# Kernel tuning notes

Measured on AMD Instinct MI355X. Metric: run time of the kernel, lower is better.

Reference implementation:

```python
import jax, jax.numpy as jnp
import numpy as np

B, N, M, D, H, K, V = 2, 2048, 2048, 1024, 16, 64, 64
MAX_WAVELENGTH = 10000
SCALE_FACTOR = 1.0


def rope(x, positions, max_wavelength, scale_factor):
    # x: [b, s, h, k]; positions: [b, s] int
    head_dim = x.shape[-1]
    fraction = 2.0 * jnp.arange(head_dim // 2, dtype=x.dtype) / head_dim
    timescale = jnp.asarray(max_wavelength, x.dtype) ** fraction            # [k/2]
    # scaled positions -> phase per (b, s, 1 head bcast, k/2)
    phase = (positions.astype(x.dtype) / scale_factor)[:, :, None, None] / timescale  # [b,s,1,k/2]
    sin, cos = jnp.sin(phase), jnp.cos(phase)
    x1, x2 = jnp.split(x, 2, axis=-1)
    return jnp.concatenate([x1 * cos - x2 * sin, x2 * cos + x1 * sin], axis=-1)


def setup_inputs() -> dict:
    key = jax.random.key(0)
    ks = jax.random.split(key, 8)
    scale = 1.0 / np.sqrt(D)  # keep logits numerically sane with random params
    inp = {
        "query": jax.random.normal(ks[0], (B, N, D), jnp.float32),
        "q_positions": jnp.broadcast_to(jnp.arange(N, dtype=jnp.int32), (B, N)),
        "key": jax.random.normal(ks[1], (B, M, D), jnp.float32),
        "k_positions": jnp.broadcast_to(jnp.arange(M, dtype=jnp.int32), (B, M)),
        "value": jax.random.normal(ks[2], (B, M, D), jnp.float32),
        "mask": jnp.ones((1, 1, N, M), dtype=bool),
        "P_q": jax.random.normal(ks[3], (H, D, K), jnp.float32) * scale,
        "P_k": jax.random.normal(ks[4], (H, D, K), jnp.float32) * scale,
        "P_v": jax.random.normal(ks[5], (H, D, V), jnp.float32) * scale,
        "P_o": jax.random.normal(ks[6], (H, D, V), jnp.float32) * scale,
    }
    return inp


def reference(query, q_positions, key, k_positions, value, mask, P_q, P_k, P_v, P_o):
    q = jnp.einsum('bnd,hdk->bnhk', query, P_q)
    k = jnp.einsum('bmd,hdk->bmhk', key, P_k)
    v = jnp.einsum('bmd,hdv->bmhv', value, P_v)
    q = rope(q, q_positions, MAX_WAVELENGTH, SCALE_FACTOR)
    k = rope(k, k_positions, MAX_WAVELENGTH, SCALE_FACTOR)
    logits = jnp.einsum('bnhk,bmhk->bhnm', q, k)
    if mask is not None:
        logits = jnp.where(mask, logits, -jnp.inf)
    weights = jax.nn.softmax(logits, axis=-1)
    o = jnp.einsum('bhnm,bmhv->bnhv', weights, v)
    return jnp.einsum('bnhv,hdv->bnd', o, P_o)
```

## Files before the change

### kernel.cpp

```cpp
#include <hip/hip_runtime.h>
#include <hip/hip_bf16.h>
#include <math.h>

#define B_ 2
#define N_ 2048
#define M_ 2048
#define D_ 1024
#define H_ 16


typedef _Float16 f16;
typedef f16  f16x4 __attribute__((ext_vector_type(4)));
typedef f16  f16x8 __attribute__((ext_vector_type(8)));
typedef float f32x4  __attribute__((ext_vector_type(4)));
typedef float f32x16 __attribute__((ext_vector_type(16)));

#define MFMA16(a, b, c) __builtin_amdgcn_mfma_f32_16x16x32_f16((a), (b), (c), 0, 0, 0)
#define MFMA32(a, b, c) __builtin_amdgcn_mfma_f32_32x32x16_f16((a), (b), (c), 0, 0, 0)
#define LDST 72

static __device__ __forceinline__ unsigned int pk2(float a, float b) {
  auto h = __builtin_amdgcn_cvt_pkrtz(a, b);
  return __builtin_bit_cast(unsigned int, h);
}

__global__ __launch_bounds__(256) void prep_all(
    const float* __restrict__ Pq, const float* __restrict__ Pk,
    const float* __restrict__ Pv, const float* __restrict__ Po,
    const int* __restrict__ qpos, const int* __restrict__ kpos,
    f16* __restrict__ Ptq, f16* __restrict__ Ptk, f16* __restrict__ Ptv,
    f16* __restrict__ Wo, float2* __restrict__ tabq, float2* __restrict__ tabk)
{
  __shared__ float Ts[64][65];
  const int z = blockIdx.y, x = blockIdx.x, tid = threadIdx.x;
  if (z < 3) {
    if (x >= 256) return;
    const float* P = (z == 0) ? Pq : (z == 1) ? Pk : Pv;
    f16* Pt = (z == 0) ? Ptq : (z == 1) ? Ptk : Ptv;
    const int d0 = (x & 15) * 64, h = x >> 4;
    #pragma unroll
    for (int it = 0; it < 4; ++it) {
      int fi = tid + 256 * it;
      int dr = fi >> 4, c4 = (fi & 15) << 2;
      float4 v = *(const float4*)(P + ((size_t)h * D_ + d0 + dr) * 64 + c4);
      Ts[dr][c4+0] = v.x; Ts[dr][c4+1] = v.y; Ts[dr][c4+2] = v.z; Ts[dr][c4+3] = v.w;
    }
    __syncthreads();
    const int c = tid >> 2, dp = (tid & 3) * 16;
    f16x8 w0, w1;
    #pragma unroll
    for (int i = 0; i < 8; ++i) { w0[i] = (f16)Ts[dp + i][c]; w1[i] = (f16)Ts[dp + 8 + i][c]; }
    f16* dst = Pt + ((size_t)h * 64 + c) * D_ + d0 + dp;
    *(f16x8*)dst = w0;
    *(f16x8*)(dst + 8) = w1;
  } else if (z == 3) {
    int e = (x * 256 + tid) * 4;
    if (e >= H_ * D_ * 64) return;
    int h = e >> 16, d = (e >> 6) & 1023, v = e & 63;
    float4 xx = *(const float4*)(Po + e);
    f16x4 w = {(f16)xx.x, (f16)xx.y, (f16)xx.z, (f16)xx.w};
    *(f16x4*)&Wo[(size_t)d * 1024 + h * 64 + v] = w;
  } else {
    if (x >= 512) return;
    int idx = x * 256 + tid;
    int r = idx >> 5, c = idx & 31;
    const int* pos = (z == 4) ? qpos : kpos;
    float2* tab = (z == 4) ? tabq : tabk;
    float fpos = (float)pos[r];
    float inv_ts = exp2f(-(float)c * 0.4152410118609203f);
    float ph = fpos * inv_ts, sn, cs;
    sincosf(ph, &sn, &cs);
    tab[idx] = make_float2(cs, sn);
  }
}

__global__ __launch_bounds__(256) void gemm_fused(
    const float* __restrict__ Aq, const float* __restrict__ Ak,
    const float* __restrict__ Av,
    const f16* __restrict__ Bq, const f16* __restrict__ Bk,
    const f16* __restrict__ Bv,
    const float2* __restrict__ tabq, const float2* __restrict__ tabk,
    f16* __restrict__ dq, f16* __restrict__ dk, f16* __restrict__ dv)
{
  __shared__ f16 As[128 * LDST];
  __shared__ f16 Bs[128 * LDST];
  const int tid = threadIdx.x, lane = tid & 63, wave = tid >> 6;
  const int quad = lane >> 4, l16 = lane & 15;
  const int lb = blockIdx.x + 8 * (int)blockIdx.y;
  const int xcd = lb & 7, t = lb >> 3;
  const int col0 = (t & 7) * 128;
  const int row0 = (xcd * 4 + (t >> 3)) * 128;
  const int op = blockIdx.z;
  const int wr = (wave >> 1) * 64, wc = (wave & 1) * 64;

  const float* A  = (op == 0) ? Aq : (op == 1) ? Ak : Av;
  const f16*  Bt  = (op == 0) ? Bq : (op == 1) ? Bk : Bv;

  f32x4 acc[4][4] = {};
  float4 apre[8];
  f16x8  bpre[4];

  #pragma unroll
  for (int it = 0; it < 8; ++it) {
    int fi = tid + 256 * it;
    int row = fi >> 4, c4 = (fi & 15) << 2;
    apre[it] = *(const float4*)(A + (size_t)(row0 + row) * 1024 + c4);
  }
  #pragma unroll
  for (int it = 0; it < 4; ++it) {
    int fi = tid + 256 * it;
    int row = fi >> 3, c8 = (fi & 7) * 8;
    bpre[it] = *(const f16x8*)(Bt + (size_t)(col0 + row) * 1024 + c8);
  }

  for (int k0 = 0; k0 < 1024; k0 += 64) {
    __syncthreads();
    #pragma unroll
    for (int it = 0; it < 8; ++it) {
      int fi = tid + 256 * it;
      int row = fi >> 4, c4 = (fi & 15) << 2;
      f16x4 hv = {(f16)apre[it].x, (f16)apre[it].y, (f16)apre[it].z, (f16)apre[it].w};
      *(f16x4*)&As[row * LDST + c4] = hv;
    }
    #pragma unroll
    for (int it = 0; it < 4; ++it) {
      int fi = tid + 256 * it;
      int row = fi >> 3, c8 = (fi & 7) * 8;
      *(f16x8*)&Bs[row * LDST + c8] = bpre[it];
    }
    __syncthreads();
    if (k0 + 64 < 1024) {
      #pragma unroll
      for (int it = 0; it < 8; ++it) {
        int fi = tid + 256 * it;
        int row = fi >> 4, c4 = (fi & 15) << 2;
        apre[it] = *(const float4*)(A + (size_t)(row0 + row) * 1024 + k0 + 64 + c4);
      }
      #pragma unroll
      for (int it = 0; it < 4; ++it) {
        int fi = tid + 256 * it;
        int row = fi >> 3, c8 = (fi & 7) * 8;
        bpre[it] = *(const f16x8*)(Bt + (size_t)(col0 + row) * 1024 + k0 + 64 + c8);
      }
    }
    #pragma unroll
    for (int ks = 0; ks < 2; ++ks) {
      f16x8 af[4], bf[4];
      #pragma unroll
      for (int i = 0; i < 4; ++i)
        af[i] = *(const f16x8*)&As[(wr + i * 16 + l16) * LDST + ks * 32 + quad * 8];
      #pragma unroll
      for (int j = 0; j < 4; ++j)
        bf[j] = *(const f16x8*)&Bs[(wc + j * 16 + l16) * LDST + ks * 32 + quad * 8];
      #pragma unroll
      for (int i = 0; i < 4; ++i)
        #pragma unroll
        for (int j = 0; j < 4; ++j)
          acc[i][j] = MFMA16(af[i], bf[j], acc[i][j]);
    }
  }

  if (op == 2) {
    #pragma unroll
    for (int i = 0; i < 4; ++i) {
      int r = row0 + wr + i * 16 + quad * 4;
      int b = r >> 11, s = r & 2047;
      #pragma unroll
      for (int j = 0; j < 4; ++j) {
        int col = col0 + wc + j * 16 + l16;
        int h = col >> 6, v = col & 63;
        f16x4 w = {(f16)acc[i][j][0], (f16)acc[i][j][1],
                   (f16)acc[i][j][2], (f16)acc[i][j][3]};
        *(f16x4*)&dv[((size_t)(b * H_ + h) * 64 + v) * 2048 + s] = w;
      }
    }
  } else {
    const float2* tab = (op == 0) ? tabq : tabk;
    f16* oq = (op == 0) ? dq : dk;
    #pragma unroll
    for (int i = 0; i < 4; ++i) {
      #pragma unroll
      for (int reg = 0; reg < 4; ++reg) {
        int r = row0 + wr + i * 16 + quad * 4 + reg;
        int b = r >> 11, s = r & 2047;
        #pragma unroll
        for (int j = 0; j < 2; ++j) {
          int col = col0 + wc + j * 16 + l16;
          int h = col >> 6, c = col & 63;
          float2 cs = tab[r * 32 + c];
          float x1 = acc[i][j][reg], x2 = acc[i][j + 2][reg];
          size_t base = ((size_t)(b * H_ + h) * 2048 + s) * 64;
          oq[base + c]      = (f16)(x1 * cs.x - x2 * cs.y);
          oq[base + c + 32] = (f16)(x2 * cs.x + x1 * cs.y);
        }
      }
    }
  }
}

__global__ __launch_bounds__(512, 4) void flash7(
    const f16* __restrict__ q, const f16* __restrict__ k,
    const f16* __restrict__ vt, f16* __restrict__ o)
{
  __shared__ __align__(16) char smem[4 * 64 * LDST * sizeof(f16)];

  const int tid = threadIdx.x, lane = tid & 63, wave = tid >> 6;
  const int g = wave >> 2, w4 = wave & 3;
  const int L = lane >> 5, nl = lane & 31;
  const int lin = blockIdx.x + 16 * (blockIdx.y + 16 * (int)blockIdx.z);
  const int xcd = lin & 7, t = lin >> 3;
  const int hb = xcd * 4 + (t >> 4);
  const int n0 = (t & 15) * 128;
  const int h = hb & 15, b = hb >> 4;

  f16* Ks  = (f16*)smem + (size_t)g * (64 * LDST);
  f16* Vts = (f16*)smem + (size_t)(2 + g) * (64 * LDST);

  const f16* qb = q  + (size_t)(b * H_ + h) * N_ * 64;
  const f16* kb = k  + (size_t)(b * H_ + h) * M_ * 64 + (size_t)g * 1024 * 64;
  const f16* vb = vt + (size_t)(b * H_ + h) * 64 * M_ + g * 1024;

  f16x8 qf[4];
  #pragma unroll
  for (int gg = 0; gg < 4; ++gg)
    qf[gg] = *(const f16x8*)(qb + (size_t)(n0 + w4 * 32 + nl) * 64 + gg * 16 + L * 8);

  f32x16 acc[2] = {};
  float mst = -INFINITY;
  float lst = 0.f;
  const float L2E = 1.4426950408889634f;

  const int gtid = tid & 255;
  const int srow = gtid >> 2, soff = (gtid & 3) * 16;

  f16x8 kp0 = *(const f16x8*)(kb + (size_t)srow * 64 + soff);
  f16x8 kp1 = *(const f16x8*)(kb + (size_t)srow * 64 + soff + 8);
  f16x8 vp0 = *(const f16x8*)(vb + (size_t)srow * M_ + soff);
  f16x8 vp1 = *(const f16x8*)(vb + (size_t)srow * M_ + soff + 8);

  for (int m0 = 0; m0 < 1024; m0 += 64) {
    __syncthreads();
    *(f16x8*)&Ks[srow * LDST + soff]      = kp0;
    *(f16x8*)&Ks[srow * LDST + soff + 8]  = kp1;
    *(f16x8*)&Vts[srow * LDST + soff]     = vp0;
    *(f16x8*)&Vts[srow * LDST + soff + 8] = vp1;
    __syncthreads();
    if (m0 + 64 < 1024) {
      kp0 = *(const f16x8*)(kb + (size_t)(m0 + 64 + srow) * 64 + soff);
      kp1 = *(const f16x8*)(kb + (size_t)(m0 + 64 + srow) * 64 + soff + 8);
      vp0 = *(const f16x8*)(vb + (size_t)srow * M_ + m0 + 64 + soff);
      vp1 = *(const f16x8*)(vb + (size_t)srow * M_ + m0 + 64 + soff + 8);
    }

    f32x16 s[2] = {};
    __builtin_amdgcn_s_setprio(1);
    #pragma unroll
    for (int u = 0; u < 2; ++u)
      #pragma unroll
      for (int gg = 0; gg < 4; ++gg) {
        f16x8 af = *(const f16x8*)&Ks[(u * 32 + nl) * LDST + gg * 16 + L * 8];
        s[u] = MFMA32(af, qf[gg], s[u]);
      }
    __builtin_amdgcn_s_setprio(0);

    float tm[16];
    #pragma unroll
    for (int r = 0; r < 16; ++r) tm[r] = fmaxf(s[0][r], s[1][r]);
    #pragma unroll
    for (int st = 8; st >= 1; st >>= 1)
      #pragma unroll
      for (int r = 0; r < st; ++r) tm[r] = fmaxf(tm[r], tm[r + st]);
    float mx = fmaxf(tm[0], __shfl_xor(tm[0], 32));
    float mx2 = mx * L2E;
    float m_new = fmaxf(mst, mx2);

    if (!__all(mx2 - mst <= 8.0f)) {
      float alpha = exp2f(mst - m_new);
      #pragma unroll
      for (int u = 0; u < 2; ++u)
        #pragma unroll
        for (int r = 0; r < 16; ++r) acc[u][r] *= alpha;
      lst *= alpha;
      mst = m_new;
    }

    float p[2][16];
    #pragma unroll
    for (int u = 0; u < 2; ++u)
      #pragma unroll
      for (int r = 0; r < 16; ++r)
        p[u][r] = exp2f(s[u][r] * L2E - mst);

    float ts[16];
    #pragma unroll
    for (int r = 0; r < 16; ++r) ts[r] = p[0][r] + p[1][r];
    #pragma unroll
    for (int st = 8; st >= 1; st >>= 1)
      #pragma unroll
      for (int r = 0; r < st; ++r) ts[r] += ts[r + st];
    float sum = ts[0];
    sum += __shfl_xor(sum, 32);
    lst += sum;

    unsigned int qw[2][4][2];
    #pragma unroll
    for (int u = 0; u < 2; ++u)
      #pragma unroll
      for (int rq = 0; rq < 4; ++rq) {
        qw[u][rq][0] = pk2(p[u][rq * 4 + 0], p[u][rq * 4 + 1]);
        qw[u][rq][1] = pk2(p[u][rq * 4 + 2], p[u][rq * 4 + 3]);
      }
    union PBu { unsigned int w[4]; f16x8 v; } pb[4];
    #pragma unroll
    for (int u = 0; u < 2; ++u)
      #pragma unroll
      for (int gg = 0; gg < 2; ++gg)
        #pragma unroll
        for (int w = 0; w < 2; ++w) {
          unsigned int a = qw[u][2 * gg][w], bb = qw[u][2 * gg + 1][w];
          asm volatile("v_permlane32_swap_b32 %0, %1" : "+v"(a), "+v"(bb));
          pb[2 * u + gg].w[w]     = a;
          pb[2 * u + gg].w[2 + w] = bb;
        }

    __builtin_amdgcn_s_setprio(1);
    #pragma unroll
    for (int u = 0; u < 2; ++u)
      #pragma unroll
      for (int gg = 0; gg < 4; ++gg) {
        f16x8 vf = *(const f16x8*)&Vts[(u * 32 + nl) * LDST + gg * 16 + L * 8];
        acc[u] = MFMA32(vf, pb[gg].v, acc[u]);
      }
    __builtin_amdgcn_s_setprio(0);
  }

  float* mrg = (float*)smem;
  const int mb = (w4 * 64 + lane) * 34;
  __syncthreads();
  if (g == 1) {
    #pragma unroll
    for (int r = 0; r < 16; ++r) { mrg[mb + r] = acc[0][r]; mrg[mb + 16 + r] = acc[1][r]; }
    mrg[mb + 32] = mst;
    mrg[mb + 33] = lst;
  }
  __syncthreads();
  if (g == 0) {
    float m1 = mrg[mb + 32], l1 = mrg[mb + 33];
    float Mm = fmaxf(mst, m1);
    float a0 = exp2f(mst - Mm), a1 = exp2f(m1 - Mm);
    float invl = 1.0f / (a0 * lst + a1 * l1);
    f16* ob = o + ((size_t)(b * N_ + n0 + w4 * 32 + nl) * 1024) + h * 64;
    #pragma unroll
    for (int u = 0; u < 2; ++u)
      #pragma unroll
      for (int rq = 0; rq < 4; ++rq) {
        f16x4 w;
        #pragma unroll
        for (int j = 0; j < 4; ++j)
          w[j] = (f16)((a0 * acc[u][rq * 4 + j] + a1 * mrg[mb + u * 16 + rq * 4 + j]) * invl);
        *(f16x4*)&ob[u * 32 + 8 * rq + 4 * L] = w;
      }
  }
}

__global__ __launch_bounds__(256) void gemm_out(
    const f16* __restrict__ A, const f16* __restrict__ Bt,
    float* __restrict__ out)
{
  __shared__ f16 As[128 * LDST];
  __shared__ f16 Bs[64 * LDST];
  const int tid = threadIdx.x, lane = tid & 63, wave = tid >> 6;
  const int quad = lane >> 4, l16 = lane & 15;
  const int lb = blockIdx.x + 16 * (int)blockIdx.y;
  const int xcd = lb & 7, t = lb >> 3;
  const int col0 = (t & 15) * 64;
  const int row0 = (xcd * 4 + (t >> 4)) * 128;
  const int wr = (wave >> 1) * 64, wc = (wave & 1) * 32;

  f32x4 acc[4][2] = {};
  f16x8 apre[4], bpre[2];

  #pragma unroll
  for (int it = 0; it < 4; ++it) {
    int fi = tid + 256 * it;
    int row = fi >> 3, c8 = (fi & 7) * 8;
    apre[it] = *(const f16x8*)(A + (size_t)(row0 + row) * 1024 + c8);
  }
  #pragma unroll
  for (int it = 0; it < 2; ++it) {
    int fi = tid + 256 * it;
    int row = fi >> 3, c8 = (fi & 7) * 8;
    bpre[it] = *(const f16x8*)(Bt + (size_t)(col0 + row) * 1024 + c8);
  }

  for (int k0 = 0; k0 < 1024; k0 += 64) {
    __syncthreads();
    #pragma unroll
    for (int it = 0; it < 4; ++it) {
      int fi = tid + 256 * it;
      int row = fi >> 3, c8 = (fi & 7) * 8;
      *(f16x8*)&As[row * LDST + c8] = apre[it];
    }
    #pragma unroll
    for (int it = 0; it < 2; ++it) {
      int fi = tid + 256 * it;
      int row = fi >> 3, c8 = (fi & 7) * 8;
      *(f16x8*)&Bs[row * LDST + c8] = bpre[it];
    }
    __syncthreads();
    if (k0 + 64 < 1024) {
      #pragma unroll
      for (int it = 0; it < 4; ++it) {
        int fi = tid + 256 * it;
        int row = fi >> 3, c8 = (fi & 7) * 8;
        apre[it] = *(const f16x8*)(A + (size_t)(row0 + row) * 1024 + k0 + 64 + c8);
      }
      #pragma unroll
      for (int it = 0; it < 2; ++it) {
        int fi = tid + 256 * it;
        int row = fi >> 3, c8 = (fi & 7) * 8;
        bpre[it] = *(const f16x8*)(Bt + (size_t)(col0 + row) * 1024 + k0 + 64 + c8);
      }
    }
    #pragma unroll
    for (int ks = 0; ks < 2; ++ks) {
      f16x8 af[4], bf[2];
      #pragma unroll
      for (int i = 0; i < 4; ++i)
        af[i] = *(const f16x8*)&As[(wr + i * 16 + l16) * LDST + ks * 32 + quad * 8];
      #pragma unroll
      for (int j = 0; j < 2; ++j)
        bf[j] = *(const f16x8*)&Bs[(wc + j * 16 + l16) * LDST + ks * 32 + quad * 8];
      #pragma unroll
      for (int i = 0; i < 4; ++i)
        #pragma unroll
        for (int j = 0; j < 2; ++j)
          acc[i][j] = MFMA16(af[i], bf[j], acc[i][j]);
    }
  }

  #pragma unroll
  for (int i = 0; i < 4; ++i)
    #pragma unroll
    for (int j = 0; j < 2; ++j)
      #pragma unroll
      for (int reg = 0; reg < 4; ++reg)
        out[(size_t)(row0 + wr + i * 16 + quad * 4 + reg) * 1024 +
            col0 + wc + j * 16 + l16] = acc[i][j][reg];
}

extern "C" void kernel_launch(void* const* d_in, const int* in_sizes, int n_in,
                              void* d_out, int out_size, void* d_ws, size_t ws_size,
                              hipStream_t stream) {
  (void)in_sizes; (void)n_in; (void)out_size; (void)ws_size;
  const float* query = (const float*)d_in[0];
  const int*   qpos  = (const int*)d_in[1];
  const float* key   = (const float*)d_in[2];
  const int*   kpos  = (const int*)d_in[3];
  const float* value = (const float*)d_in[4];
  const float* Pq = (const float*)d_in[6];
  const float* Pk = (const float*)d_in[7];
  const float* Pv = (const float*)d_in[8];
  const float* Po = (const float*)d_in[9];
  float* out = (float*)d_out;

  const size_t pm = (size_t)1024 * 1024;
  const size_t em = (size_t)B_ * H_ * 2048 * 64;
  f16* Ptq = (f16*)d_ws;
  f16* Ptk = Ptq + pm;
  f16* Ptv = Ptk + pm;
  f16* Wo  = Ptv + pm;
  f16* q_ws  = Wo + pm;
  f16* k_ws  = q_ws + em;
  f16* vt_ws = k_ws + em;
  f16* o_ws  = vt_ws + em;
  float2* tabq = (float2*)(o_ws + em);
  float2* tabk = tabq + (size_t)4096 * 32;

  dim3 blk(256);
  prep_all<<<dim3(1024, 6), blk, 0, stream>>>(
      Pq, Pk, Pv, Po, qpos, kpos, Ptq, Ptk, Ptv, Wo, tabq, tabk);

  gemm_fused<<<dim3(8, 32, 3), blk, 0, stream>>>(
      query, key, value, Ptq, Ptk, Ptv, tabq, tabk, q_ws, k_ws, vt_ws);

  flash7<<<dim3(N_ / 128, H_, B_), dim3(512), 0, stream>>>(q_ws, k_ws, vt_ws, o_ws);

  gemm_out<<<dim3(16, 32), blk, 0, stream>>>(o_ws, Wo, out);
}
```

Measured before the change: 249.1 us.

## Load K/V fragments directly from global memory, dropping LDS staging and syncs

```diff
diff --git a/kernel.cpp b/kernel.cpp
--- a/kernel.cpp
+++ b/kernel.cpp
@@ -18,6 +18,7 @@
 #define MFMA16(a, b, c) __builtin_amdgcn_mfma_f32_16x16x32_f16((a), (b), (c), 0, 0, 0)
 #define MFMA32(a, b, c) __builtin_amdgcn_mfma_f32_32x32x16_f16((a), (b), (c), 0, 0, 0)
 #define LDST 72
+#define EXP2(x) __builtin_amdgcn_exp2f(x)
 
 static __device__ __forceinline__ unsigned int pk2(float a, float b) {
   auto h = __builtin_amdgcn_cvt_pkrtz(a, b);
@@ -198,23 +199,20 @@
   }
 }
 
-__global__ __launch_bounds__(512, 4) void flash7(
+__global__ __launch_bounds__(256, 3) void flash9(
     const f16* __restrict__ q, const f16* __restrict__ k,
     const f16* __restrict__ vt, f16* __restrict__ o)
 {
-  __shared__ __align__(16) char smem[4 * 64 * LDST * sizeof(f16)];
+  __shared__ float mrg[2 * 64 * 34];
 
   const int tid = threadIdx.x, lane = tid & 63, wave = tid >> 6;
-  const int g = wave >> 2, w4 = wave & 3;
+  const int g = wave >> 1, w2 = wave & 1;
   const int L = lane >> 5, nl = lane & 31;
-  const int lin = blockIdx.x + 16 * (blockIdx.y + 16 * (int)blockIdx.z);
+  const int lin = blockIdx.x;
   const int xcd = lin & 7, t = lin >> 3;
-  const int hb = xcd * 4 + (t >> 4);
-  const int n0 = (t & 15) * 128;
+  const int hb = xcd * 4 + (t >> 5);
+  const int n0 = (t & 31) * 64;
   const int h = hb & 15, b = hb >> 4;
-
-  f16* Ks  = (f16*)smem + (size_t)g * (64 * LDST);
-  f16* Vts = (f16*)smem + (size_t)(2 + g) * (64 * LDST);
 
   const f16* qb = q  + (size_t)(b * H_ + h) * N_ * 64;
   const f16* kb = k  + (size_t)(b * H_ + h) * M_ * 64 + (size_t)g * 1024 * 64;
@@ -223,45 +221,35 @@
   f16x8 qf[4];
   #pragma unroll
   for (int gg = 0; gg < 4; ++gg)
-    qf[gg] = *(const f16x8*)(qb + (size_t)(n0 + w4 * 32 + nl) * 64 + gg * 16 + L * 8);
+    qf[gg] = *(const f16x8*)(qb + (size_t)(n0 + w2 * 32 + nl) * 64 + gg * 16 + L * 8);
 
   f32x16 acc[2] = {};
   float mst = -INFINITY;
   float lst = 0.f;
   const float L2E = 1.4426950408889634f;
 
-  const int gtid = tid & 255;
-  const int srow = gtid >> 2, soff = (gtid & 3) * 16;
-
-  f16x8 kp0 = *(const f16x8*)(kb + (size_t)srow * 64 + soff);
-  f16x8 kp1 = *(const f16x8*)(kb + (size_t)srow * 64 + soff + 8);
-  f16x8 vp0 = *(const f16x8*)(vb + (size_t)srow * M_ + soff);
-  f16x8 vp1 = *(const f16x8*)(vb + (size_t)srow * M_ + soff + 8);
-
   for (int m0 = 0; m0 < 1024; m0 += 64) {
-    __syncthreads();
-    *(f16x8*)&Ks[srow * LDST + soff]      = kp0;
-    *(f16x8*)&Ks[srow * LDST + soff + 8]  = kp1;
-    *(f16x8*)&Vts[srow * LDST + soff]     = vp0;
-    *(f16x8*)&Vts[srow * LDST + soff + 8] = vp1;
-    __syncthreads();
-    if (m0 + 64 < 1024) {
-      kp0 = *(const f16x8*)(kb + (size_t)(m0 + 64 + srow) * 64 + soff);
-      kp1 = *(const f16x8*)(kb + (size_t)(m0 + 64 + srow) * 64 + soff + 8);
-      vp0 = *(const f16x8*)(vb + (size_t)srow * M_ + m0 + 64 + soff);
-      vp1 = *(const f16x8*)(vb + (size_t)srow * M_ + m0 + 64 + soff + 8);
-    }
-
+    f16x8 kf0[4], kf1[4];
+    #pragma unroll
+    for (int gg = 0; gg < 4; ++gg) {
+      kf0[gg] = *(const f16x8*)(kb + (size_t)(m0 + nl) * 64 + gg * 16 + L * 8);
+      kf1[gg] = *(const f16x8*)(kb + (size_t)(m0 + 32 + nl) * 64 + gg * 16 + L * 8);
+    }
     f32x16 s[2] = {};
     __builtin_amdgcn_s_setprio(1);
     #pragma unroll
-    for (int u = 0; u < 2; ++u)
-      #pragma unroll
-      for (int gg = 0; gg < 4; ++gg) {
-        f16x8 af = *(const f16x8*)&Ks[(u * 32 + nl) * LDST + gg * 16 + L * 8];
-        s[u] = MFMA32(af, qf[gg], s[u]);
-      }
+    for (int gg = 0; gg < 4; ++gg) {
+      s[0] = MFMA32(kf0[gg], qf[gg], s[0]);
+      s[1] = MFMA32(kf1[gg], qf[gg], s[1]);
+    }
     __builtin_amdgcn_s_setprio(0);
+
+    f16x8 vf0[4], vf1[4];
+    #pragma unroll
+    for (int gg = 0; gg < 4; ++gg) {
+      vf0[gg] = *(const f16x8*)(vb + (size_t)nl * M_ + m0 + gg * 16 + L * 8);
+      vf1[gg] = *(const f16x8*)(vb + (size_t)(32 + nl) * M_ + m0 + gg * 16 + L * 8);
+    }
 
     float tm[16];
     #pragma unroll
@@ -275,7 +263,7 @@
     float m_new = fmaxf(mst, mx2);
 
     if (!__all(mx2 - mst <= 8.0f)) {
-      float alpha = exp2f(mst - m_new);
+      float alpha = EXP2(mst - m_new);
       #pragma unroll
       for (int u = 0; u < 2; ++u)
         #pragma unroll
@@ -284,16 +272,15 @@
       mst = m_new;
     }
 
-    float p[2][16];
     #pragma unroll
     for (int u = 0; u < 2; ++u)
       #pragma unroll
       for (int r = 0; r < 16; ++r)
-        p[u][r] = exp2f(s[u][r] * L2E - mst);
+        s[u][r] = EXP2(s[u][r] * L2E - mst);
 
     float ts[16];
     #pragma unroll
-    for (int r = 0; r < 16; ++r) ts[r] = p[0][r] + p[1][r];
+    for (int r = 0; r < 16; ++r) ts[r] = s[0][r] + s[1][r];
     #pragma unroll
     for (int st = 8; st >= 1; st >>= 1)
       #pragma unroll
@@ -307,8 +294,8 @@
     for (int u = 0; u < 2; ++u)
       #pragma unroll
       for (int rq = 0; rq < 4; ++rq) {
-        qw[u][rq][0] = pk2(p[u][rq * 4 + 0], p[u][rq * 4 + 1]);
-        qw[u][rq][1] = pk2(p[u][rq * 4 + 2], p[u][rq * 4 + 3]);
+        qw[u][rq][0] = pk2(s[u][rq * 4 + 0], s[u][rq * 4 + 1]);
+        qw[u][rq][1] = pk2(s[u][rq * 4 + 2], s[u][rq * 4 + 3]);
       }
     union PBu { unsigned int w[4]; f16x8 v; } pb[4];
     #pragma unroll
@@ -325,17 +312,14 @@
 
     __builtin_amdgcn_s_setprio(1);
     #pragma unroll
-    for (int u = 0; u < 2; ++u)
-      #pragma unroll
-      for (int gg = 0; gg < 4; ++gg) {
-        f16x8 vf = *(const f16x8*)&Vts[(u * 32 + nl) * LDST + gg * 16 + L * 8];
-        acc[u] = MFMA32(vf, pb[gg].v, acc[u]);
-      }
+    for (int gg = 0; gg < 4; ++gg) {
+      acc[0] = MFMA32(vf0[gg], pb[gg].v, acc[0]);
+      acc[1] = MFMA32(vf1[gg], pb[gg].v, acc[1]);
+    }
     __builtin_amdgcn_s_setprio(0);
   }
 
-  float* mrg = (float*)smem;
-  const int mb = (w4 * 64 + lane) * 34;
+  const int mb = (w2 * 64 + lane) * 34;
   __syncthreads();
   if (g == 1) {
     #pragma unroll
@@ -347,9 +331,9 @@
   if (g == 0) {
     float m1 = mrg[mb + 32], l1 = mrg[mb + 33];
     float Mm = fmaxf(mst, m1);
-    float a0 = exp2f(mst - Mm), a1 = exp2f(m1 - Mm);
+    float a0 = EXP2(mst - Mm), a1 = EXP2(m1 - Mm);
     float invl = 1.0f / (a0 * lst + a1 * l1);
-    f16* ob = o + ((size_t)(b * N_ + n0 + w4 * 32 + nl) * 1024) + h * 64;
+    f16* ob = o + ((size_t)(b * N_ + n0 + w2 * 32 + nl) * 1024) + h * 64;
     #pragma unroll
     for (int u = 0; u < 2; ++u)
       #pragma unroll
@@ -484,7 +468,7 @@
   gemm_fused<<<dim3(8, 32, 3), blk, 0, stream>>>(
       query, key, value, Ptq, Ptk, Ptv, tabq, tabk, q_ws, k_ws, vt_ws);
 
-  flash7<<<dim3(N_ / 128, H_, B_), dim3(512), 0, stream>>>(q_ws, k_ws, vt_ws, o_ws);
+  flash9<<<dim3(1024), blk, 0, stream>>>(q_ws, k_ws, vt_ws, o_ws);
 
   gemm_out<<<dim3(16, 32), blk, 0, stream>>>(o_ws, Wo, out);
 }
```

Result: slower. 309.4 us (+24.2%).
